# Performance work log

Measured on AMD Instinct MI355X. Metric: run time of the kernel, lower is better.

## Reference

```python
import jax, jax.numpy as jnp
import numpy as np

N_NODES = 100000
N_EDGES = 1_600_000
D_IN = 128
D_OUT = 128


def setup_inputs() -> dict:
    key = jax.random.key(0)
    k_x, k_w, k_col, k_row = jax.random.split(key, 4)
    X = jax.random.normal(k_x, (N_NODES, D_IN), dtype=jnp.float32)
    weights = jax.random.normal(k_w, (D_IN, D_OUT), dtype=jnp.float32) * (1.0 / np.sqrt(D_OUT))
    # edge list: destination rows sorted (CSR order), random source columns
    edgeToRow = jnp.sort(jax.random.randint(k_row, (N_EDGES,), 0, N_NODES, dtype=jnp.int32))
    column_index = jax.random.randint(k_col, (N_EDGES,), 0, N_NODES, dtype=jnp.int32)
    # row_pointers consistent with edgeToRow
    row_np = np.asarray(edgeToRow)
    row_pointers = jnp.asarray(np.searchsorted(row_np, np.arange(N_NODES + 1)), dtype=jnp.int32)
    # TC-GNN-style tiling metadata (layout only; does not affect math)
    n_windows = (N_NODES + 15) // 16
    blockPartition = jnp.ones((n_windows,), dtype=jnp.int32)
    edgeToColumn = jnp.zeros((N_EDGES,), dtype=jnp.int32)
    hybrid_type = jnp.zeros((n_windows,), dtype=jnp.int32)
    row_nzr = jnp.zeros((n_windows + 1,), dtype=jnp.int32)
    col_nzr = jnp.zeros((N_NODES,), dtype=jnp.int32)
    return {
        "X": X,
        "weights": weights,
        "row_pointers": row_pointers,
        "column_index": column_index,
        "blockPartition": blockPartition,
        "edgeToColumn": edgeToColumn,
        "edgeToRow": edgeToRow,
        "hybrid_type": hybrid_type,
        "row_nzr": row_nzr,
        "col_nzr": col_nzr,
    }


def reference(X, weights, row_pointers, column_index, blockPartition,
              edgeToColumn, edgeToRow, hybrid_type, row_nzr, col_nzr):
    # Fused SpMM aggregation (A @ X with implicit unit edge values) + dense GEMM.
    # blockPartition/edgeToColumn/hybrid_type/row_nzr/col_nzr are kernel layout
    # metadata and do not change the math.
    gathered = jnp.take(X, column_index, axis=0)                  # [E, D_IN]
    X_prime = jax.ops.segment_sum(gathered, edgeToRow,
                                  num_segments=X.shape[0])        # [N, D_IN]
    return X_prime @ weights                                      # [N, D_OUT]
```

## Files before the change

### kernel.cpp

```cpp
#include <hip/hip_runtime.h>
#include <hip/hip_bf16.h>

typedef short short8 __attribute__((ext_vector_type(8)));
typedef float floatx4 __attribute__((ext_vector_type(4)));
typedef unsigned int uintx4 __attribute__((ext_vector_type(4)));
typedef unsigned int uintx2 __attribute__((ext_vector_type(2)));

__device__ __forceinline__ unsigned short f2bf_u(float f) {
    __hip_bfloat16 h = __float2bfloat16(f);
    return *reinterpret_cast<unsigned short*>(&h);
}

__device__ __forceinline__ float bflo(unsigned u) {
    unsigned l = u << 16;
    return __builtin_bit_cast(float, l);
}
__device__ __forceinline__ float bfhi(unsigned u) {
    unsigned h = u & 0xffff0000u;
    return __builtin_bit_cast(float, h);
}
__device__ __forceinline__ void acc_u4(floatx4& A, floatx4& B, uintx4 u) {
    A.x += bflo(u.x); A.y += bfhi(u.x);
    A.z += bflo(u.y); A.w += bfhi(u.y);
    B.x += bflo(u.z); B.y += bfhi(u.z);
    B.z += bflo(u.w); B.w += bfhi(u.w);
}

__global__ void wprep_kernel(const float* __restrict__ W,
                             __hip_bfloat16* __restrict__ Wt) {
    int tid = blockIdx.x * blockDim.x + threadIdx.x;
    int n = tid & 127;
    int k = tid >> 7;
    Wt[n * 128 + k] = __float2bfloat16(W[k * 128 + n]);
}

__global__ __launch_bounds__(256)
void gemm_kernel(const float* __restrict__ X,
                 const __hip_bfloat16* __restrict__ Wt,
                 char* __restrict__ Yb) {
    __shared__ unsigned short As[32 * 128];

    int tid = threadIdx.x;
    size_t rowbase = (size_t)blockIdx.x * 32;

    {
        int rr = tid >> 5;
        int c4 = (tid & 31) * 4;
        int kb = c4 >> 3;
        int ko = c4 & 7;
#pragma unroll
        for (int it = 0; it < 4; ++it) {
            int row = it * 8 + rr;
            floatx4 f = __builtin_nontemporal_load(
                (const floatx4*)(X + (rowbase + row) * 128 + c4));
            uintx2 p;
            p.x = (unsigned)f2bf_u(f.x) | ((unsigned)f2bf_u(f.y) << 16);
            p.y = (unsigned)f2bf_u(f.z) | ((unsigned)f2bf_u(f.w) << 16);
            *(uintx2*)(As + row * 128 + ((kb ^ (row & 15)) << 3) + ko) = p;
        }
    }
    __syncthreads();

    int wv   = tid >> 6;
    int lane = tid & 63;
    int m16  = lane & 15;
    int quad = lane >> 4;
    int rt   = wv & 1;
    int ctb  = (wv >> 1) * 4;

    floatx4 acc[4] = {{0,0,0,0},{0,0,0,0},{0,0,0,0},{0,0,0,0}};
    int arow = rt * 16 + m16;
#pragma unroll
    for (int s = 0; s < 4; ++s) {
        int kb = quad + s * 4;
        short8 bfrag = *(const short8*)(As + arow * 128 + ((kb ^ m16) << 3));
#pragma unroll
        for (int t = 0; t < 4; ++t) {
            short8 afrag = *(const short8*)(Wt + ((ctb + t) * 16 + m16) * 128 +
                                            quad * 8 + s * 32);
            acc[t] = __builtin_amdgcn_mfma_f32_16x16x32_bf16(afrag, bfrag,
                                                             acc[t], 0, 0, 0);
        }
    }

    size_t orow = rowbase + rt * 16 + m16;
#pragma unroll
    for (int t = 0; t < 4; ++t) {
        int ocol = (ctb + t) * 16 + quad * 4;
        uintx2 p;
        p.x = (unsigned)f2bf_u(acc[t][0]) | ((unsigned)f2bf_u(acc[t][1]) << 16);
        p.y = (unsigned)f2bf_u(acc[t][2]) | ((unsigned)f2bf_u(acc[t][3]) << 16);
        *(uintx2*)(Yb + orow * 256 + ocol * 2) = p;
    }
}

__global__ __launch_bounds__(256)
void agg_kernel(const char* __restrict__ Yb,
                const int* __restrict__ row_pointers,
                const int* __restrict__ column_index,
                float* __restrict__ out) {
    int tid  = threadIdx.x;
    int lane = tid & 63;
    int r    = blockIdx.x * 4 + (tid >> 6);
    int sub  = lane >> 4;
    int fo   = (lane & 15) * 16;

    int e0 = row_pointers[r];
    int e1 = row_pointers[r + 1];

    floatx4 accA = {0.f, 0.f, 0.f, 0.f};
    floatx4 accB = {0.f, 0.f, 0.f, 0.f};

    int e = e0;
    int elast = e0 + ((e1 - e0) & ~15);
    for (; e < elast; e += 16) {
        int c0 = column_index[e + sub];
        int c1 = column_index[e + 4 + sub];
        int c2 = column_index[e + 8 + sub];
        int c3 = column_index[e + 12 + sub];
        uintx4 u0 = *(const uintx4*)(Yb + (size_t)c0 * 256 + fo);
        uintx4 u1 = *(const uintx4*)(Yb + (size_t)c1 * 256 + fo);
        uintx4 u2 = *(const uintx4*)(Yb + (size_t)c2 * 256 + fo);
        uintx4 u3 = *(const uintx4*)(Yb + (size_t)c3 * 256 + fo);
        acc_u4(accA, accB, u0);
        acc_u4(accA, accB, u1);
        acc_u4(accA, accB, u2);
        acc_u4(accA, accB, u3);
    }
    if (e < e1) {
#pragma unroll
        for (int g = 0; g < 4; ++g) {
            int idx = e + g * 4 + sub;
            if (idx < e1) {
                int c = column_index[idx];
                uintx4 u = *(const uintx4*)(Yb + (size_t)c * 256 + fo);
                acc_u4(accA, accB, u);
            }
        }
    }

#pragma unroll
    for (int m = 16; m <= 32; m <<= 1) {
        accA.x += __shfl_xor(accA.x, m);
        accA.y += __shfl_xor(accA.y, m);
        accA.z += __shfl_xor(accA.z, m);
        accA.w += __shfl_xor(accA.w, m);
        accB.x += __shfl_xor(accB.x, m);
        accB.y += __shfl_xor(accB.y, m);
        accB.z += __shfl_xor(accB.z, m);
        accB.w += __shfl_xor(accB.w, m);
    }

    if (sub == 0) {
        float* dst = out + (size_t)r * 128 + (lane & 15) * 8;
        __builtin_nontemporal_store(accA, (floatx4*)dst);
        __builtin_nontemporal_store(accB, (floatx4*)(dst + 4));
    }
}

extern "C" void kernel_launch(void* const* d_in, const int* in_sizes, int n_in,
                              void* d_out, int out_size, void* d_ws, size_t ws_size,
                              hipStream_t stream) {
    const float* X       = (const float*)d_in[0];
    const float* W       = (const float*)d_in[1];
    const int* row_ptrs  = (const int*)d_in[2];
    const int* col_index = (const int*)d_in[3];

    float* out = (float*)d_out;
    const int N = in_sizes[2] - 1;

    char* ws = (char*)d_ws;
    __hip_bfloat16* Wt = (__hip_bfloat16*)ws;
    char* Yb = ws + 32768;

    wprep_kernel<<<64, 256, 0, stream>>>(W, Wt);
    gemm_kernel<<<N / 32, 256, 0, stream>>>(X, Wt, Yb);
    agg_kernel<<<N / 4, 256, 0, stream>>>(Yb, row_ptrs, col_index, out);
}
```

Baseline: 209.5 us.

## Aggregate 16 rows per block with LDS-staged column indices

Each block now handles 16 destination rows, one 16-lane group per row, and stages the block's column indices in shared memory before gathering. The cross-lane shuffle reduction is removed because each group owns whole rows, and the inner loop issues 8 independent gathers per iteration. This cuts global index loads and the shuffle reduction cost. In exchange it adds a block-wide barrier and LDS usage, and gives less memory parallelism per row since a row's edges are walked by only 16 lanes, which may increase load imbalance across rows.

New measurement: 210.0 us. No clear change (+0.3%).

```diff
diff --git a/kernel.cpp b/kernel.cpp
--- a/kernel.cpp
+++ b/kernel.cpp
@@ -99,63 +99,84 @@
                 const int* __restrict__ row_pointers,
                 const int* __restrict__ column_index,
                 float* __restrict__ out) {
-    int tid  = threadIdx.x;
-    int lane = tid & 63;
-    int r    = blockIdx.x * 4 + (tid >> 6);
-    int sub  = lane >> 4;
-    int fo   = (lane & 15) * 16;
-
-    int e0 = row_pointers[r];
-    int e1 = row_pointers[r + 1];
+    constexpr int CAP = 2048;
+    __shared__ int colS[CAP];
+    __shared__ int rpS[17];
+
+    int tid = threadIdx.x;
+    int R = blockIdx.x * 16;
+    if (tid < 17) rpS[tid] = row_pointers[R + tid];
+    __syncthreads();
+
+    int eblk0 = rpS[0];
+    int cnt = rpS[16] - eblk0;
+    int stage = cnt < CAP ? cnt : CAP;
+    for (int i = tid; i < stage; i += 256)
+        colS[i] = column_index[eblk0 + i];
+    __syncthreads();
+
+    int g  = tid >> 4;
+    int l  = tid & 15;
+    int fo = l * 16;
+    int r  = R + g;
+    int e0 = rpS[g];
+    int e1 = rpS[g + 1];
 
     floatx4 accA = {0.f, 0.f, 0.f, 0.f};
     floatx4 accB = {0.f, 0.f, 0.f, 0.f};
 
-    int e = e0;
-    int elast = e0 + ((e1 - e0) & ~15);
-    for (; e < elast; e += 16) {
-        int c0 = column_index[e + sub];
-        int c1 = column_index[e + 4 + sub];
-        int c2 = column_index[e + 8 + sub];
-        int c3 = column_index[e + 12 + sub];
-        uintx4 u0 = *(const uintx4*)(Yb + (size_t)c0 * 256 + fo);
-        uintx4 u1 = *(const uintx4*)(Yb + (size_t)c1 * 256 + fo);
-        uintx4 u2 = *(const uintx4*)(Yb + (size_t)c2 * 256 + fo);
-        uintx4 u3 = *(const uintx4*)(Yb + (size_t)c3 * 256 + fo);
-        acc_u4(accA, accB, u0);
-        acc_u4(accA, accB, u1);
-        acc_u4(accA, accB, u2);
-        acc_u4(accA, accB, u3);
-    }
-    if (e < e1) {
-#pragma unroll
-        for (int g = 0; g < 4; ++g) {
-            int idx = e + g * 4 + sub;
+    if (e1 - eblk0 <= CAP) {
+        int i = e0;
+        int end8 = e0 + ((e1 - e0) & ~7);
+        for (; i < end8; i += 8) {
+            int k = i - eblk0;
+            int c0 = colS[k + 0], c1 = colS[k + 1];
+            int c2 = colS[k + 2], c3 = colS[k + 3];
+            int c4 = colS[k + 4], c5 = colS[k + 5];
+            int c6 = colS[k + 6], c7 = colS[k + 7];
+            uintx4 u0 = *(const uintx4*)(Yb + (size_t)c0 * 256 + fo);
+            uintx4 u1 = *(const uintx4*)(Yb + (size_t)c1 * 256 + fo);
+            uintx4 u2 = *(const uintx4*)(Yb + (size_t)c2 * 256 + fo);
+            uintx4 u3 = *(const uintx4*)(Yb + (size_t)c3 * 256 + fo);
+            uintx4 u4 = *(const uintx4*)(Yb + (size_t)c4 * 256 + fo);
+            uintx4 u5 = *(const uintx4*)(Yb + (size_t)c5 * 256 + fo);
+            uintx4 u6 = *(const uintx4*)(Yb + (size_t)c6 * 256 + fo);
+            uintx4 u7 = *(const uintx4*)(Yb + (size_t)c7 * 256 + fo);
+            acc_u4(accA, accB, u0);
+            acc_u4(accA, accB, u1);
+            acc_u4(accA, accB, u2);
+            acc_u4(accA, accB, u3);
+            acc_u4(accA, accB, u4);
+            acc_u4(accA, accB, u5);
+            acc_u4(accA, accB, u6);
+            acc_u4(accA, accB, u7);
+        }
+#pragma unroll
+        for (int j = 0; j < 7; ++j) {
+            int idx = i + j;
             if (idx < e1) {
-                int c = column_index[idx];
+                int c = colS[idx - eblk0];
                 uintx4 u = *(const uintx4*)(Yb + (size_t)c * 256 + fo);
                 acc_u4(accA, accB, u);
             }
         }
-    }
-
-#pragma unroll
-    for (int m = 16; m <= 32; m <<= 1) {
-        accA.x += __shfl_xor(accA.x, m);
-        accA.y += __shfl_xor(accA.y, m);
-        accA.z += __shfl_xor(accA.z, m);
-        accA.w += __shfl_xor(accA.w, m);
-        accB.x += __shfl_xor(accB.x, m);
-        accB.y += __shfl_xor(accB.y, m);
-        accB.z += __shfl_xor(accB.z, m);
-        accB.w += __shfl_xor(accB.w, m);
-    }
-
-    if (sub == 0) {
-        float* dst = out + (size_t)r * 128 + (lane & 15) * 8;
-        __builtin_nontemporal_store(accA, (floatx4*)dst);
-        __builtin_nontemporal_store(accB, (floatx4*)(dst + 4));
-    }
+    } else {
+        for (int i = e0; i < e1; i += 4) {
+#pragma unroll
+            for (int j = 0; j < 4; ++j) {
+                int idx = i + j;
+                if (idx < e1) {
+                    int c = column_index[idx];
+                    uintx4 u = *(const uintx4*)(Yb + (size_t)c * 256 + fo);
+                    acc_u4(accA, accB, u);
+                }
+            }
+        }
+    }
+
+    float* dst = out + (size_t)r * 128 + l * 8;
+    __builtin_nontemporal_store(accA, (floatx4*)dst);
+    __builtin_nontemporal_store(accB, (floatx4*)(dst + 4));
 }
 
 extern "C" void kernel_launch(void* const* d_in, const int* in_sizes, int n_in,
@@ -175,5 +196,5 @@
 
     wprep_kernel<<<64, 256, 0, stream>>>(W, Wt);
     gemm_kernel<<<N / 32, 256, 0, stream>>>(X, Wt, Yb);
-    agg_kernel<<<N / 4, 256, 0, stream>>>(Yb, row_ptrs, col_index, out);
-}
+    agg_kernel<<<N / 16, 256, 0, stream>>>(Yb, row_ptrs, col_index, out);
+}
```
